# Kernel tuning notes

Measured on AMD Instinct MI355X. Metric: run time of the kernel, lower is better.

The kernel has to match this reference:

```python
import jax, jax.numpy as jnp
import numpy as np

R, DIL = 3, 2  # radius, dilation for neighbor correlation


def conv2d(x, w, b):
    # standard 3x3 stride-1 SAME conv, NCHW / OIHW
    y = jax.lax.conv_general_dilated(x, w, (1, 1), 'SAME',
                                     dimension_numbers=('NCHW', 'OIHW', 'NCHW'))
    return y + b[None, :, None, None]


def bilinear_gather(x, py, px):
    # x: (n,c,h,w); py/px: (n,K,h,w) float sampling coords; zero outside bounds
    n, c, h, w = x.shape
    y0 = jnp.floor(py); x0 = jnp.floor(px)
    wy = py - y0; wx = px - x0
    xf = x.reshape(n, c, h * w)

    def gather(yi, xi):
        valid = ((yi >= 0) & (yi < h) & (xi >= 0) & (xi < w)).astype(x.dtype)
        yc = jnp.clip(yi, 0, h - 1).astype(jnp.int32)
        xc = jnp.clip(xi, 0, w - 1).astype(jnp.int32)
        idx = (yc * w + xc).reshape(n, -1)  # (n, K*h*w)
        v = jax.vmap(lambda f, i: f[:, i])(xf, idx)  # (n, c, K*h*w)
        return v.reshape(n, c, *yi.shape[1:]) * valid[:, None]

    v00 = gather(y0, x0); v01 = gather(y0, x0 + 1)
    v10 = gather(y0 + 1, x0); v11 = gather(y0 + 1, x0 + 1)
    wy_ = wy[:, None]; wx_ = wx[:, None]
    return (v00 * (1 - wy_) * (1 - wx_) + v01 * (1 - wy_) * wx_
            + v10 * wy_ * (1 - wx_) + v11 * wy_ * wx_)


def dcn(x, w, b, ow, ob):
    # DCNv2-style modulated deformable 3x3 conv, stride 1, pad 1, 1 deformable group.
    # Offset/mask predicted by an internal conv: channels = [dy(9), dx(9), mask(9)].
    n, c, h, w_ = x.shape
    K = 9
    om = conv2d(x, ow, ob)  # (n, 27, h, w)
    dy, dx = om[:, :K], om[:, K:2 * K]
    mask = jax.nn.sigmoid(om[:, 2 * K:])
    ky, kx = jnp.meshgrid(jnp.arange(-1, 2), jnp.arange(-1, 2), indexing='ij')
    ky = ky.reshape(K).astype(x.dtype); kx = kx.reshape(K).astype(x.dtype)
    yy = jnp.arange(h, dtype=x.dtype)[None, None, :, None]
    xx = jnp.arange(w_, dtype=x.dtype)[None, None, None, :]
    py = yy + ky[None, :, None, None] + dy  # (n,K,h,w)
    px = xx + kx[None, :, None, None] + dx
    samp = bilinear_gather(x, py, px) * mask[:, None]  # (n,c,K,h,w)
    return jnp.einsum('nckhw,ock->nohw', samp, w.reshape(w.shape[0], c, K)) + b[None, :, None, None]


def ncf(f1, f2, radius, dilation):
    # neighbor_correlation_filter: unfold-based sliding-window dot-product attention
    n, c, h, w = f2.shape
    k = 2 * radius + 1
    pad = (k - 1) * dilation // 2
    f2p = jnp.pad(f2, ((0, 0), (0, 0), (pad, pad), (pad, pad)))
    # (n,c,K,h,w), tap order (ky outer, kx inner) matching F.unfold row-major layout
    patches = jnp.stack([f2p[:, :, i * dilation:i * dilation + h, j * dilation:j * dilation + w]
                         for i in range(k) for j in range(k)], axis=2)
    corr = jnp.einsum('nchw,nckhw->nkhw', f1, patches) / jnp.sqrt(jnp.asarray(c, f1.dtype))
    attn = jax.nn.softmax(corr, axis=1)
    sample = jnp.einsum('nkhw,nckhw->nchw', attn, patches)
    return sample, corr


def stargru(x, t, zw, zb, zow, zob, hw, hb, how, hob):
    tx = jnp.concatenate([x, t], axis=1)
    z = jax.nn.sigmoid(dcn(tx, zw, zb, zow, zob))
    r, _ = ncf(t, x, R, DIL)
    xt = jnp.tanh(dcn(jnp.concatenate([r, t], axis=1), hw, hb, how, hob))
    return (1.0 - z) * t + z * xt


def setup_inputs():
    key = jax.random.key(0)
    N, CIN, CH, H, W = 2, 256, 64, 96, 96
    ks = iter(jax.random.split(key, 32))

    def rn(shape, s=0.05):
        return jax.random.normal(next(ks), shape, jnp.float32) * s

    inp = {
        'x': jax.random.normal(next(ks), (N, CIN, H, W), jnp.float32),
        'template': jax.random.normal(next(ks), (N, CH, H, W), jnp.float32),
        'w_in': rn((CH, CIN, 3, 3)), 'b_in': jnp.zeros((CH,), jnp.float32),
        'w_out': rn((CIN, CH, 3, 3)), 'b_out': jnp.zeros((CIN,), jnp.float32),
    }
    for pre in ('enh_z', 'enh_h', 'upd_z', 'upd_h'):
        inp[pre + '_w'] = rn((CH, 2 * CH, 3, 3))
        inp[pre + '_b'] = jnp.zeros((CH,), jnp.float32)
        inp[pre + '_ow'] = rn((27, 2 * CH, 3, 3), 0.01)  # offset/mask conv (small init)
        inp[pre + '_ob'] = jnp.zeros((27,), jnp.float32)
    return inp


def reference(x, template, w_in, b_in, w_out, b_out,
              enh_z_w, enh_z_b, enh_z_ow, enh_z_ob,
              enh_h_w, enh_h_b, enh_h_ow, enh_h_ob,
              upd_z_w, upd_z_b, upd_z_ow, upd_z_ob,
              upd_h_w, upd_h_b, upd_h_ow, upd_h_ob):
    # CrossUpdate forward, post-first-frame branch (self.template is not None)
    xh = conv2d(x, w_in, b_in)
    x_enh = stargru(template, xh,
                    enh_z_w, enh_z_b, enh_z_ow, enh_z_ob,
                    enh_h_w, enh_h_b, enh_h_ow, enh_h_ob)
    new_template = stargru(xh, template,
                           upd_z_w, upd_z_b, upd_z_ow, upd_z_ob,
                           upd_h_w, upd_h_b, upd_h_ow, upd_h_ob)
    out = conv2d(x_enh, w_out, b_out)
    return (out, new_template)
```

## Files before the change

kernel.cpp:

```cpp
#include <hip/hip_runtime.h>
#include <hip/hip_bf16.h>

typedef __hip_bfloat16 bf16;
typedef unsigned short u16;
typedef unsigned int u32;
typedef __attribute__((ext_vector_type(8))) short short8;
typedef __attribute__((ext_vector_type(4))) short bh4;
typedef __attribute__((ext_vector_type(4))) float floatx4;

constexpr int N_ = 2, H_ = 96, W_ = 96, HW_ = H_ * W_;
constexpr int CIN_ = 256, CH_ = 64, C2_ = 128;

__device__ __forceinline__ float sigm(float v) { return 1.0f / (1.0f + __expf(-v)); }
__device__ __forceinline__ short f2b(float v) { bf16 h = __float2bfloat16(v); return *reinterpret_cast<short*>(&h); }
__device__ __forceinline__ float b2f(short s) {
    union { u32 i; float f; } v; v.i = ((u32)(u16)s) << 16; return v.f;
}

constexpr int A_IN_OFF = 0,                         A_IN_SZ  = 64 * 2304;
constexpr int A_OUT_OFF = A_IN_OFF + A_IN_SZ,       A_OUT_SZ = 256 * 576;
constexpr int A_OFF_OFF = A_OUT_OFF + A_OUT_SZ,     A_OFF_SZ = 64 * 1152;
constexpr int A_DCN_OFF = A_OFF_OFF + 4 * A_OFF_SZ, A_DCN_SZ = 64 * 1152;
constexpr int A_TOT = A_DCN_OFF + 4 * A_DCN_SZ;

__global__ __launch_bounds__(256) void cvt_weights(
        const float* __restrict__ w_in, const float* __restrict__ w_out,
        const float* __restrict__ ow0, const float* __restrict__ ow1,
        const float* __restrict__ ow2, const float* __restrict__ ow3,
        const float* __restrict__ w0, const float* __restrict__ w1,
        const float* __restrict__ w2, const float* __restrict__ w3,
        u16* __restrict__ dst) {
    int id = blockIdx.x * 256 + threadIdx.x;
    if (id >= A_TOT) return;
    float v;
    if (id < A_OUT_OFF) {
        int l = id; int m = l / 2304, k = l % 2304; int tap = k >> 8, ic = k & 255;
        v = w_in[m * 2304 + ic * 9 + tap];
    } else if (id < A_OFF_OFF) {
        int l = id - A_OUT_OFF; int m = l / 576, k = l % 576; int tap = k / 64, ic = k & 63;
        v = w_out[m * 576 + ic * 9 + tap];
    } else if (id < A_DCN_OFF) {
        int l = id - A_OFF_OFF; int i = l / A_OFF_SZ, l2 = l % A_OFF_SZ;
        int m = l2 / 1152, k = l2 % 1152; int tap = k >> 7, ic = k & 127;
        const float* s = (i == 0) ? ow0 : (i == 1) ? ow1 : (i == 2) ? ow2 : ow3;
        v = (m < 27) ? s[m * 1152 + ic * 9 + tap] : 0.f;
    } else {
        int l = id - A_DCN_OFF; int i = l / A_DCN_SZ, l2 = l % A_DCN_SZ;
        int m = l2 / 1152, k = l2 % 1152; int tap = k >> 7, c = k & 127;
        const float* s = (i == 0) ? w0 : (i == 1) ? w1 : (i == 2) ? w2 : w3;
        v = s[m * 1152 + c * 9 + tap];
    }
    short sb = f2b(v);
    dst[id] = *reinterpret_cast<u16*>(&sb);
}

__global__ __launch_bounds__(256) void to_nhwc(const float* __restrict__ src, u16* __restrict__ dst, int C) {
    int id = blockIdx.x * 256 + threadIdx.x;
    int c8n = C >> 3;
    if (id >= N_ * HW_ * c8n) return;
    int c8 = id % c8n;
    int pix = id / c8n;
    int n = pix / HW_, p = pix % HW_;
    const float* s = src + ((size_t)n * C + c8 * 8) * HW_ + p;
    short8 vv;
#pragma unroll
    for (int j = 0; j < 8; ++j) vv[j] = f2b(s[(size_t)j * HW_]);
    *reinterpret_cast<short8*>(dst + (size_t)pix * C + c8 * 8) = vv;
}

__global__ __launch_bounds__(256) void concat_dual(const float* __restrict__ tpl, const float* __restrict__ xh,
                                                   u16* __restrict__ ta, u16* __restrict__ tb) {
    int id = blockIdx.x * 256 + threadIdx.x;
    if (id >= N_ * HW_ * 16) return;
    int c8 = id & 15;
    int pix = id >> 4;
    int n = pix / HW_, p = pix % HW_;
    int c = c8 * 8;
    const float* s = (c < 64) ? tpl + ((size_t)n * 64 + c) * HW_ + p
                              : xh + ((size_t)n * 64 + (c - 64)) * HW_ + p;
    short8 vv;
#pragma unroll
    for (int j = 0; j < 8; ++j) vv[j] = f2b(s[(size_t)j * HW_]);
    *reinterpret_cast<short8*>(ta + (size_t)pix * 128 + c) = vv;
    *reinterpret_cast<short8*>(tb + (size_t)pix * 128 + ((c + 64) & 127)) = vv;
}

template <int IC, int OCST>
__device__ __forceinline__ void conv_core(const u16* __restrict__ X,
                                          const u16* __restrict__ A,
                                          const float* __restrict__ bias,
                                          float* __restrict__ out,
                                          int r, int mt, int t) {
    constexpr int K = IC * 9;
    constexpr int ICC = IC / 64;
    __shared__ __align__(16) u16 Xl[3][50][72];
    int n = r / 192;
    int rr = r % 192;
    int y = rr >> 1, px0 = (rr & 1) * 48;
    int w = t >> 6, lane = t & 63, lm = lane & 15, q = lane >> 4;
    const u16* Arow = A + (size_t)(mt * 64 + w * 16 + lm) * K + q * 8;
    floatx4 acc[3];
#pragma unroll
    for (int a = 0; a < 3; ++a) acc[a] = {0.f, 0.f, 0.f, 0.f};
    const short8 zz = {0, 0, 0, 0, 0, 0, 0, 0};

    for (int icc = 0; icc < ICC; ++icc) {
        short8 af[9][2];
#pragma unroll
        for (int tap = 0; tap < 9; ++tap)
#pragma unroll
            for (int ks = 0; ks < 2; ++ks)
                af[tap][ks] = *reinterpret_cast<const short8*>(Arow + tap * IC + icc * 64 + ks * 32);
        __syncthreads();
#pragma unroll
        for (int it = 0; it < 5; ++it) {
            int id = it * 256 + t;
            if (id < 1200) {
                int ch8 = id & 7;
                int tmp = id >> 3;
                int pxl = tmp % 50, row = tmp / 50;
                int xg = px0 - 1 + pxl;
                int yg = y - 1 + row;
                bool vld = (yg >= 0) && (yg < 96) && (xg >= 0) && (xg < 96);
                short8 vv = zz;
                if (vld)
                    vv = *reinterpret_cast<const short8*>(
                        X + ((size_t)(n * HW_ + yg * 96 + xg)) * IC + icc * 64 + ch8 * 8);
                *reinterpret_cast<short8*>(&Xl[row][pxl][ch8 * 8]) = vv;
            }
        }
        __syncthreads();
#pragma unroll
        for (int tap = 0; tap < 9; ++tap) {
            int ky = tap / 3, kx = tap % 3;
#pragma unroll
            for (int ks = 0; ks < 2; ++ks) {
#pragma unroll
                for (int nf = 0; nf < 3; ++nf) {
                    short8 bv = *reinterpret_cast<const short8*>(&Xl[ky][nf * 16 + lm + kx][ks * 32 + q * 8]);
                    acc[nf] = __builtin_amdgcn_mfma_f32_16x16x32_bf16(af[tap][ks], bv, acc[nf], 0, 0, 0);
                }
            }
        }
    }
    int ocb = mt * 64 + w * 16 + q * 4;
#pragma unroll
    for (int nf = 0; nf < 3; ++nf) {
        int px = px0 + nf * 16 + lm;
#pragma unroll
        for (int rr2 = 0; rr2 < 4; ++rr2) {
            int oc = ocb + rr2;
            if (oc < OCST)
                out[((size_t)(n * OCST + oc)) * HW_ + y * 96 + px] = acc[nf][rr2] + bias[oc];
        }
    }
}

template <int IC, int OCST>
__global__ __launch_bounds__(256) void conv_gemm(const u16* __restrict__ X,
                                                 const u16* __restrict__ A,
                                                 const float* __restrict__ bias,
                                                 float* __restrict__ out) {
    conv_core<IC, OCST>(X, A, bias, out, blockIdx.x % 384, blockIdx.x / 384, threadIdx.x);
}

__global__ __launch_bounds__(256) void conv_gemm2(const u16* __restrict__ X0, const u16* __restrict__ X1,
                                                  const u16* __restrict__ A0, const u16* __restrict__ A1,
                                                  const float* __restrict__ b0, const float* __restrict__ b1,
                                                  float* __restrict__ o0, float* __restrict__ o1) {
    int inst = blockIdx.x / 384, r = blockIdx.x % 384;
    conv_core<C2_, 27>(inst ? X1 : X0, inst ? A1 : A0, inst ? b1 : b0, inst ? o1 : o0, r, 0, threadIdx.x);
}

__device__ __forceinline__ void dcn_core(const u16* __restrict__ txh,
                                         const float* __restrict__ om,
                                         const u16* __restrict__ A,
                                         const float* __restrict__ bias,
                                         float* __restrict__ out,
                                         int r, int t) {
    __shared__ __align__(16) u16 Bl[48][72];
    __shared__ float s_wy[432], s_wx[432], s_m[432];
    __shared__ int s_y0[432], s_x0[432];
    int n = r / 192;
    int rr = r % 192;
    int y = rr >> 1, px0 = (rr & 1) * 48;
    for (int e = t; e < 432; e += 256) {
        int k9 = e / 48, xl = e % 48;
        int x = px0 + xl;
        const float* ob = om + (size_t)n * 27 * HW_ + y * 96 + x;
        float dy = ob[(size_t)k9 * HW_];
        float dx = ob[(size_t)(9 + k9) * HW_];
        float ml = ob[(size_t)(18 + k9) * HW_];
        float py = (float)y + (float)(k9 / 3 - 1) + dy;
        float px = (float)x + (float)(k9 % 3 - 1) + dx;
        float fy = floorf(py), fx = floorf(px);
        s_y0[e] = (int)fy; s_x0[e] = (int)fx;
        s_wy[e] = py - fy; s_wx[e] = px - fx; s_m[e] = sigm(ml);
    }
    int w = t >> 6, lane = t & 63, lm = lane & 15, q = lane >> 4;
    const u16* Arow = A + (size_t)(w * 16 + lm) * 1152 + q * 8;
    floatx4 acc[3];
#pragma unroll
    for (int a = 0; a < 3; ++a) acc[a] = {0.f, 0.f, 0.f, 0.f};
    const u16* txn = txh + (size_t)n * HW_ * 128;
    const short8 zz = {0, 0, 0, 0, 0, 0, 0, 0};

    for (int kc = 0; kc < 18; ++kc) {
        int tap = kc >> 1, c0 = (kc & 1) * 64;
        short8 af[2];
#pragma unroll
        for (int ks = 0; ks < 2; ++ks)
            af[ks] = *reinterpret_cast<const short8*>(Arow + kc * 64 + ks * 32);
        __syncthreads();
#pragma unroll
        for (int i = 0; i < 2; ++i) {
            int id = i * 256 + t;
            if (id < 384) {
                int px = id >> 3, ch8 = id & 7;
                int ce = tap * 48 + px;
                int y0 = s_y0[ce], x0 = s_x0[ce];
                float wy = s_wy[ce], wx = s_wx[ce], m = s_m[ce];
                float w00 = (1.f - wy) * (1.f - wx) * m;
                float w01 = (1.f - wy) * wx * m;
                float w10 = wy * (1.f - wx) * m;
                float w11 = wy * wx * m;
                bool yv0 = (y0 >= 0) & (y0 < 96), yv1 = (y0 >= -1) & (y0 < 95);
                bool xv0 = (x0 >= 0) & (x0 < 96), xv1 = (x0 >= -1) & (x0 < 95);
                const u16* base = txn + (long)(y0 * 96 + x0) * 128 + c0 + ch8 * 8;
                short8 v00 = (yv0 && xv0) ? *reinterpret_cast<const short8*>(base) : zz;
                short8 v01 = (yv0 && xv1) ? *reinterpret_cast<const short8*>(base + 128) : zz;
                short8 v10 = (yv1 && xv0) ? *reinterpret_cast<const short8*>(base + 96 * 128) : zz;
                short8 v11 = (yv1 && xv1) ? *reinterpret_cast<const short8*>(base + 96 * 128 + 128) : zz;
                short8 vv;
#pragma unroll
                for (int j = 0; j < 8; ++j) {
                    float f = b2f(v00[j]) * w00 + b2f(v01[j]) * w01 +
                              b2f(v10[j]) * w10 + b2f(v11[j]) * w11;
                    vv[j] = f2b(f);
                }
                *reinterpret_cast<short8*>(&Bl[px][ch8 * 8]) = vv;
            }
        }
        __syncthreads();
#pragma unroll
        for (int ks = 0; ks < 2; ++ks)
#pragma unroll
            for (int nf = 0; nf < 3; ++nf) {
                short8 bv = *reinterpret_cast<const short8*>(&Bl[nf * 16 + lm][ks * 32 + q * 8]);
                acc[nf] = __builtin_amdgcn_mfma_f32_16x16x32_bf16(af[ks], bv, acc[nf], 0, 0, 0);
            }
    }
    int ocb = w * 16 + q * 4;
#pragma unroll
    for (int nf = 0; nf < 3; ++nf) {
        int px = px0 + nf * 16 + lm;
#pragma unroll
        for (int rr2 = 0; rr2 < 4; ++rr2) {
            int oc = ocb + rr2;
            out[((size_t)(n * CH_ + oc)) * HW_ + y * 96 + px] = acc[nf][rr2] + bias[oc];
        }
    }
}

__global__ __launch_bounds__(256) void dcn_gemm2(const u16* __restrict__ X0, const u16* __restrict__ X1,
                                                 const float* __restrict__ om0, const float* __restrict__ om1,
                                                 const u16* __restrict__ A0, const u16* __restrict__ A1,
                                                 const float* __restrict__ b0, const float* __restrict__ b1,
                                                 float* __restrict__ o0, float* __restrict__ o1) {
    int inst = blockIdx.x / 384, r = blockIdx.x % 384;
    dcn_core(inst ? X1 : X0, inst ? om1 : om0, inst ? A1 : A0, inst ? b1 : b0, inst ? o1 : o0, r, threadIdx.x);
}

__global__ __launch_bounds__(256, 4) void ncf2(const u16* __restrict__ in0, const u16* __restrict__ in1,
                                               u16* __restrict__ out0, u16* __restrict__ out1) {
    __shared__ __align__(16) u16 sF2[7][28][72];
    __shared__ __align__(16) u16 sF1[16][72];
    __shared__ float sc[16][52];
    int t = threadIdx.x;
    int inst = blockIdx.x / 1152, bb = blockIdx.x % 1152;
    const u16* txh = inst ? in1 : in0;
    u16* txh2 = inst ? out1 : out0;
    int n = bb / 576, rem = bb % 576;
    int y = rem / 6, x0 = (rem % 6) * 16;
    const u16* base = txh + (size_t)n * HW_ * 128;
    const short8 zz = {0, 0, 0, 0, 0, 0, 0, 0};

    for (int id = t; id < 1568; id += 256) {
        int ch8 = id & 7;
        int tmp = id >> 3;
        int px = tmp % 28, row = tmp / 28;
        int yy = y + row * 2 - 6;
        int xg = x0 - 6 + px;
        short8 vv = zz;
        if (yy >= 0 && yy < 96 && xg >= 0 && xg < 96)
            vv = *reinterpret_cast<const short8*>(base + (size_t)(yy * 96 + xg) * 128 + ch8 * 8);
        *reinterpret_cast<short8*>(&sF2[row][px][ch8 * 8]) = vv;
    }
    if (t < 128) {
        int ch8 = t & 7, lp0 = t >> 3;
        short8 vv = *reinterpret_cast<const short8*>(base + (size_t)(y * 96 + x0 + lp0) * 128 + 64 + ch8 * 8);
        *reinterpret_cast<short8*>(&sF1[lp0][ch8 * 8]) = vv;
    }
    __syncthreads();

    int lp = t >> 4, j = t & 15;
    for (int k = j; k < 49; k += 16) {
        int ky = k / 7, kx = k % 7;
        const u16* f2p = &sF2[ky][lp + 2 * kx][0];
        const u16* f1p = &sF1[lp][0];
        float s = 0.f;
#pragma unroll
        for (int c8 = 0; c8 < 8; ++c8) {
            short8 a = *reinterpret_cast<const short8*>(f1p + c8 * 8);
            short8 b = *reinterpret_cast<const short8*>(f2p + c8 * 8);
#pragma unroll
            for (int u = 0; u < 8; ++u) s += b2f(a[u]) * b2f(b[u]);
        }
        sc[lp][k] = s * 0.125f;
    }
    float mx = -1e30f;
    for (int k = j; k < 49; k += 16) mx = fmaxf(mx, sc[lp][k]);
#pragma unroll
    for (int m = 1; m <= 8; m <<= 1) mx = fmaxf(mx, __shfl_xor(mx, m, 64));
    float e[4];
    float sum = 0.f;
    int cnt = 0;
    for (int k = j; k < 49; k += 16) { e[cnt] = __expf(sc[lp][k] - mx); sum += e[cnt]; ++cnt; }
#pragma unroll
    for (int m = 1; m <= 8; m <<= 1) sum += __shfl_xor(sum, m, 64);
    float inv = 1.f / sum;
    cnt = 0;
    for (int k = j; k < 49; k += 16) sc[lp][k] = e[cnt++] * inv;
    __syncthreads();
    int ch0 = j * 4;
    float acc[4];
#pragma unroll
    for (int u = 0; u < 4; ++u) acc[u] = 0.f;
#pragma unroll
    for (int k = 0; k < 49; ++k) {
        int ky = k / 7, kx = k % 7;
        float a = sc[lp][k];
        bh4 f2 = *reinterpret_cast<const bh4*>(&sF2[ky][lp + 2 * kx][ch0]);
#pragma unroll
        for (int u = 0; u < 4; ++u) acc[u] += a * b2f(f2[u]);
    }
    int p = y * 96 + x0 + lp;
    u16* obase = txh2 + (size_t)n * HW_ * 128 + (size_t)p * 128;
    bh4 ro;
#pragma unroll
    for (int u = 0; u < 4; ++u) ro[u] = f2b(acc[u]);
    *reinterpret_cast<bh4*>(obase + ch0) = ro;
    *reinterpret_cast<bh4*>(obase + 64 + ch0) =
        *reinterpret_cast<const bh4*>(&sF1[lp][ch0]);
}

__global__ __launch_bounds__(256) void gate_dual(const float* __restrict__ dz_a, const float* __restrict__ dh_a,
                                                 const float* __restrict__ t_a, u16* __restrict__ dst_a,
                                                 const float* __restrict__ dz_b, const float* __restrict__ dh_b,
                                                 const float* __restrict__ t_b, float* __restrict__ dst_b) {
    int inst = blockIdx.x / 576, bb = blockIdx.x % 576;
    int id = bb * 256 + threadIdx.x;
    int c8 = id & 7;
    int pix = id >> 3;
    int n = pix / HW_, p = pix % HW_;
    const float* zpre = inst ? dz_b : dz_a;
    const float* hpre = inst ? dh_b : dh_a;
    const float* tt = inst ? t_b : t_a;
    if (!inst) {
        short8 vv;
#pragma unroll
        for (int j = 0; j < 8; ++j) {
            size_t idx = ((size_t)n * CH_ + c8 * 8 + j) * HW_ + p;
            float z = sigm(zpre[idx]);
            float xt = tanhf(hpre[idx]);
            vv[j] = f2b((1.f - z) * tt[idx] + z * xt);
        }
        *reinterpret_cast<short8*>(dst_a + (size_t)pix * CH_ + c8 * 8) = vv;
    } else {
#pragma unroll
        for (int j = 0; j < 8; ++j) {
            size_t idx = ((size_t)n * CH_ + c8 * 8 + j) * HW_ + p;
            float z = sigm(zpre[idx]);
            float xt = tanhf(hpre[idx]);
            dst_b[idx] = (1.f - z) * tt[idx] + z * xt;
        }
    }
}

extern "C" void kernel_launch(void* const* d_in, const int* in_sizes, int n_in,
                              void* d_out, int out_size, void* d_ws, size_t ws_size,
                              hipStream_t stream) {
    const float* x     = (const float*)d_in[0];
    const float* tpl   = (const float*)d_in[1];
    const float* w_in  = (const float*)d_in[2];
    const float* b_in  = (const float*)d_in[3];
    const float* w_out = (const float*)d_in[4];
    const float* b_out = (const float*)d_in[5];
    const float *pw[4], *pb[4], *pow_[4], *pob[4];
    for (int i = 0; i < 4; ++i) {
        pw[i]   = (const float*)d_in[6 + 4 * i];
        pb[i]   = (const float*)d_in[7 + 4 * i];
        pow_[i] = (const float*)d_in[8 + 4 * i];
        pob[i]  = (const float*)d_in[9 + 4 * i];
    }
    float* out_main = (float*)d_out;
    float* out_ntpl = out_main + (size_t)N_ * CIN_ * HW_;

    u16* Aws = (u16*)d_ws;
    u16* xT     = Aws + A_TOT;
    u16* txh_a  = xT + (size_t)N_ * HW_ * CIN_;
    u16* txh_b  = txh_a + (size_t)N_ * HW_ * C2_;
    u16* txh2_a = txh_b + (size_t)N_ * HW_ * C2_;
    u16* txh2_b = txh2_a + (size_t)N_ * HW_ * C2_;
    u16* xeh    = txh2_b + (size_t)N_ * HW_ * C2_;
    float* fws = (float*)(xeh + (size_t)N_ * HW_ * CH_);
    size_t off = 0;
    float* xh   = fws + off; off += (size_t)N_ * CH_ * HW_;
    float* om_a = fws + off; off += (size_t)N_ * 27 * HW_;
    float* om_b = fws + off; off += (size_t)N_ * 27 * HW_;
    float* dz_a = fws + off; off += (size_t)N_ * CH_ * HW_;
    float* dz_b = fws + off; off += (size_t)N_ * CH_ * HW_;
    float* dh_a = fws + off; off += (size_t)N_ * CH_ * HW_;
    float* dh_b = fws + off; off += (size_t)N_ * CH_ * HW_;

    cvt_weights<<<(A_TOT + 255) / 256, 256, 0, stream>>>(
        w_in, w_out, pow_[0], pow_[1], pow_[2], pow_[3], pw[0], pw[1], pw[2], pw[3], Aws);
    to_nhwc<<<2304, 256, 0, stream>>>(x, xT, CIN_);
    conv_gemm<CIN_, 64><<<384, 256, 0, stream>>>(xT, Aws + A_IN_OFF, b_in, xh);

    concat_dual<<<1152, 256, 0, stream>>>(tpl, xh, txh_a, txh_b);
    conv_gemm2<<<768, 256, 0, stream>>>(txh_a, txh_b,
        Aws + A_OFF_OFF + 0 * A_OFF_SZ, Aws + A_OFF_OFF + 2 * A_OFF_SZ, pob[0], pob[2], om_a, om_b);
    dcn_gemm2<<<768, 256, 0, stream>>>(txh_a, txh_b, om_a, om_b,
        Aws + A_DCN_OFF + 0 * A_DCN_SZ, Aws + A_DCN_OFF + 2 * A_DCN_SZ, pb[0], pb[2], dz_a, dz_b);
    ncf2<<<2304, 256, 0, stream>>>(txh_a, txh_b, txh2_a, txh2_b);
    conv_gemm2<<<768, 256, 0, stream>>>(txh2_a, txh2_b,
        Aws + A_OFF_OFF + 1 * A_OFF_SZ, Aws + A_OFF_OFF + 3 * A_OFF_SZ, pob[1], pob[3], om_a, om_b);
    dcn_gemm2<<<768, 256, 0, stream>>>(txh2_a, txh2_b, om_a, om_b,
        Aws + A_DCN_OFF + 1 * A_DCN_SZ, Aws + A_DCN_OFF + 3 * A_DCN_SZ, pb[1], pb[3], dh_a, dh_b);
    gate_dual<<<1152, 256, 0, stream>>>(dz_a, dh_a, xh, xeh, dz_b, dh_b, tpl, out_ntpl);

    conv_gemm<CH_, 256><<<1536, 256, 0, stream>>>(xeh, Aws + A_OUT_OFF, b_out, out_main);
}
```

Baseline: 344.0 us.

## Shrink conv/DCN tiles to 32 pixels and merge four offset-conv/DCN launches

The conv and DCN GEMM cores now cover 32-pixel row segments instead of 48, giving more blocks per launch and a smaller LDS footprint. The separate enhance and update offset-conv and DCN launches become one four-instance conv_quad and one dcn_quad launch, with ncf2 moved ahead so all inputs are ready. This cuts launch count and fixes under-filled grids on a large-CU GPU. In exchange, halo overhead per pixel rises (34/32 vs 50/48), weight fragment reuse per block drops, and a second pair of offset buffers is needed.

```diff
diff --git a/kernel.cpp b/kernel.cpp
--- a/kernel.cpp
+++ b/kernel.cpp
@@ -93,15 +93,15 @@
                                           int r, int mt, int t) {
     constexpr int K = IC * 9;
     constexpr int ICC = IC / 64;
-    __shared__ __align__(16) u16 Xl[3][50][72];
-    int n = r / 192;
-    int rr = r % 192;
-    int y = rr >> 1, px0 = (rr & 1) * 48;
+    __shared__ __align__(16) u16 Xl[3][34][72];
+    int n = r / 288;
+    int rr = r % 288;
+    int y = rr / 3, px0 = (rr % 3) * 32;
     int w = t >> 6, lane = t & 63, lm = lane & 15, q = lane >> 4;
     const u16* Arow = A + (size_t)(mt * 64 + w * 16 + lm) * K + q * 8;
-    floatx4 acc[3];
-#pragma unroll
-    for (int a = 0; a < 3; ++a) acc[a] = {0.f, 0.f, 0.f, 0.f};
+    floatx4 acc[2];
+#pragma unroll
+    for (int a = 0; a < 2; ++a) acc[a] = {0.f, 0.f, 0.f, 0.f};
     const short8 zz = {0, 0, 0, 0, 0, 0, 0, 0};
 
     for (int icc = 0; icc < ICC; ++icc) {
@@ -113,12 +113,12 @@
                 af[tap][ks] = *reinterpret_cast<const short8*>(Arow + tap * IC + icc * 64 + ks * 32);
         __syncthreads();
 #pragma unroll
-        for (int it = 0; it < 5; ++it) {
+        for (int it = 0; it < 4; ++it) {
             int id = it * 256 + t;
-            if (id < 1200) {
+            if (id < 816) {
                 int ch8 = id & 7;
                 int tmp = id >> 3;
-                int pxl = tmp % 50, row = tmp / 50;
+                int pxl = tmp % 34, row = tmp / 34;
                 int xg = px0 - 1 + pxl;
                 int yg = y - 1 + row;
                 bool vld = (yg >= 0) && (yg < 96) && (xg >= 0) && (xg < 96);
@@ -136,7 +136,7 @@
 #pragma unroll
             for (int ks = 0; ks < 2; ++ks) {
 #pragma unroll
-                for (int nf = 0; nf < 3; ++nf) {
+                for (int nf = 0; nf < 2; ++nf) {
                     short8 bv = *reinterpret_cast<const short8*>(&Xl[ky][nf * 16 + lm + kx][ks * 32 + q * 8]);
                     acc[nf] = __builtin_amdgcn_mfma_f32_16x16x32_bf16(af[tap][ks], bv, acc[nf], 0, 0, 0);
                 }
@@ -145,7 +145,7 @@
     }
     int ocb = mt * 64 + w * 16 + q * 4;
 #pragma unroll
-    for (int nf = 0; nf < 3; ++nf) {
+    for (int nf = 0; nf < 2; ++nf) {
         int px = px0 + nf * 16 + lm;
 #pragma unroll
         for (int rr2 = 0; rr2 < 4; ++rr2) {
@@ -161,15 +161,23 @@
                                                  const u16* __restrict__ A,
                                                  const float* __restrict__ bias,
                                                  float* __restrict__ out) {
-    conv_core<IC, OCST>(X, A, bias, out, blockIdx.x % 384, blockIdx.x / 384, threadIdx.x);
-}
-
-__global__ __launch_bounds__(256) void conv_gemm2(const u16* __restrict__ X0, const u16* __restrict__ X1,
-                                                  const u16* __restrict__ A0, const u16* __restrict__ A1,
-                                                  const float* __restrict__ b0, const float* __restrict__ b1,
-                                                  float* __restrict__ o0, float* __restrict__ o1) {
-    int inst = blockIdx.x / 384, r = blockIdx.x % 384;
-    conv_core<C2_, 27>(inst ? X1 : X0, inst ? A1 : A0, inst ? b1 : b0, inst ? o1 : o0, r, 0, threadIdx.x);
+    conv_core<IC, OCST>(X, A, bias, out, blockIdx.x % 576, blockIdx.x / 576, threadIdx.x);
+}
+
+__global__ __launch_bounds__(256) void conv_quad(const u16* __restrict__ X0, const u16* __restrict__ X1,
+                                                 const u16* __restrict__ X2, const u16* __restrict__ X3,
+                                                 const u16* __restrict__ A0, const u16* __restrict__ A1,
+                                                 const u16* __restrict__ A2, const u16* __restrict__ A3,
+                                                 const float* __restrict__ b0, const float* __restrict__ b1,
+                                                 const float* __restrict__ b2, const float* __restrict__ b3,
+                                                 float* __restrict__ o0, float* __restrict__ o1,
+                                                 float* __restrict__ o2, float* __restrict__ o3) {
+    int inst = blockIdx.x / 576, r = blockIdx.x % 576;
+    const u16* X = (inst == 0) ? X0 : (inst == 1) ? X1 : (inst == 2) ? X2 : X3;
+    const u16* A = (inst == 0) ? A0 : (inst == 1) ? A1 : (inst == 2) ? A2 : A3;
+    const float* b = (inst == 0) ? b0 : (inst == 1) ? b1 : (inst == 2) ? b2 : b3;
+    float* o = (inst == 0) ? o0 : (inst == 1) ? o1 : (inst == 2) ? o2 : o3;
+    conv_core<C2_, 27>(X, A, b, o, r, 0, threadIdx.x);
 }
 
 __device__ __forceinline__ void dcn_core(const u16* __restrict__ txh,
@@ -178,14 +186,14 @@
                                          const float* __restrict__ bias,
                                          float* __restrict__ out,
                                          int r, int t) {
-    __shared__ __align__(16) u16 Bl[48][72];
-    __shared__ float s_wy[432], s_wx[432], s_m[432];
-    __shared__ int s_y0[432], s_x0[432];
-    int n = r / 192;
-    int rr = r % 192;
-    int y = rr >> 1, px0 = (rr & 1) * 48;
-    for (int e = t; e < 432; e += 256) {
-        int k9 = e / 48, xl = e % 48;
+    __shared__ __align__(16) u16 Bl[32][72];
+    __shared__ float s_wy[288], s_wx[288], s_m[288];
+    __shared__ int s_y0[288], s_x0[288];
+    int n = r / 288;
+    int rr = r % 288;
+    int y = rr / 3, px0 = (rr % 3) * 32;
+    for (int e = t; e < 288; e += 256) {
+        int k9 = e / 32, xl = e % 32;
         int x = px0 + xl;
         const float* ob = om + (size_t)n * 27 * HW_ + y * 96 + x;
         float dy = ob[(size_t)k9 * HW_];
@@ -199,9 +207,9 @@
     }
     int w = t >> 6, lane = t & 63, lm = lane & 15, q = lane >> 4;
     const u16* Arow = A + (size_t)(w * 16 + lm) * 1152 + q * 8;
-    floatx4 acc[3];
-#pragma unroll
-    for (int a = 0; a < 3; ++a) acc[a] = {0.f, 0.f, 0.f, 0.f};
+    floatx4 acc[2];
+#pragma unroll
+    for (int a = 0; a < 2; ++a) acc[a] = {0.f, 0.f, 0.f, 0.f};
     const u16* txn = txh + (size_t)n * HW_ * 128;
     const short8 zz = {0, 0, 0, 0, 0, 0, 0, 0};
 
@@ -212,47 +220,43 @@
         for (int ks = 0; ks < 2; ++ks)
             af[ks] = *reinterpret_cast<const short8*>(Arow + kc * 64 + ks * 32);
         __syncthreads();
-#pragma unroll
-        for (int i = 0; i < 2; ++i) {
-            int id = i * 256 + t;
-            if (id < 384) {
-                int px = id >> 3, ch8 = id & 7;
-                int ce = tap * 48 + px;
-                int y0 = s_y0[ce], x0 = s_x0[ce];
-                float wy = s_wy[ce], wx = s_wx[ce], m = s_m[ce];
-                float w00 = (1.f - wy) * (1.f - wx) * m;
-                float w01 = (1.f - wy) * wx * m;
-                float w10 = wy * (1.f - wx) * m;
-                float w11 = wy * wx * m;
-                bool yv0 = (y0 >= 0) & (y0 < 96), yv1 = (y0 >= -1) & (y0 < 95);
-                bool xv0 = (x0 >= 0) & (x0 < 96), xv1 = (x0 >= -1) & (x0 < 95);
-                const u16* base = txn + (long)(y0 * 96 + x0) * 128 + c0 + ch8 * 8;
-                short8 v00 = (yv0 && xv0) ? *reinterpret_cast<const short8*>(base) : zz;
-                short8 v01 = (yv0 && xv1) ? *reinterpret_cast<const short8*>(base + 128) : zz;
-                short8 v10 = (yv1 && xv0) ? *reinterpret_cast<const short8*>(base + 96 * 128) : zz;
-                short8 v11 = (yv1 && xv1) ? *reinterpret_cast<const short8*>(base + 96 * 128 + 128) : zz;
-                short8 vv;
-#pragma unroll
-                for (int j = 0; j < 8; ++j) {
-                    float f = b2f(v00[j]) * w00 + b2f(v01[j]) * w01 +
-                              b2f(v10[j]) * w10 + b2f(v11[j]) * w11;
-                    vv[j] = f2b(f);
-                }
-                *reinterpret_cast<short8*>(&Bl[px][ch8 * 8]) = vv;
+        {
+            int px = t >> 3, ch8 = t & 7;
+            int ce = tap * 32 + px;
+            int y0 = s_y0[ce], x0 = s_x0[ce];
+            float wy = s_wy[ce], wx = s_wx[ce], m = s_m[ce];
+            float w00 = (1.f - wy) * (1.f - wx) * m;
+            float w01 = (1.f - wy) * wx * m;
+            float w10 = wy * (1.f - wx) * m;
+            float w11 = wy * wx * m;
+            bool yv0 = (y0 >= 0) & (y0 < 96), yv1 = (y0 >= -1) & (y0 < 95);
+            bool xv0 = (x0 >= 0) & (x0 < 96), xv1 = (x0 >= -1) & (x0 < 95);
+            const u16* base = txn + (long)(y0 * 96 + x0) * 128 + c0 + ch8 * 8;
+            short8 v00 = (yv0 && xv0) ? *reinterpret_cast<const short8*>(base) : zz;
+            short8 v01 = (yv0 && xv1) ? *reinterpret_cast<const short8*>(base + 128) : zz;
+            short8 v10 = (yv1 && xv0) ? *reinterpret_cast<const short8*>(base + 96 * 128) : zz;
+            short8 v11 = (yv1 && xv1) ? *reinterpret_cast<const short8*>(base + 96 * 128 + 128) : zz;
+            short8 vv;
+#pragma unroll
+            for (int j = 0; j < 8; ++j) {
+                float f = b2f(v00[j]) * w00 + b2f(v01[j]) * w01 +
+                          b2f(v10[j]) * w10 + b2f(v11[j]) * w11;
+                vv[j] = f2b(f);
             }
+            *reinterpret_cast<short8*>(&Bl[px][ch8 * 8]) = vv;
         }
         __syncthreads();
 #pragma unroll
         for (int ks = 0; ks < 2; ++ks)
 #pragma unroll
-            for (int nf = 0; nf < 3; ++nf) {
+            for (int nf = 0; nf < 2; ++nf) {
                 short8 bv = *reinterpret_cast<const short8*>(&Bl[nf * 16 + lm][ks * 32 + q * 8]);
                 acc[nf] = __builtin_amdgcn_mfma_f32_16x16x32_bf16(af[ks], bv, acc[nf], 0, 0, 0);
             }
     }
     int ocb = w * 16 + q * 4;
 #pragma unroll
-    for (int nf = 0; nf < 3; ++nf) {
+    for (int nf = 0; nf < 2; ++nf) {
         int px = px0 + nf * 16 + lm;
 #pragma unroll
         for (int rr2 = 0; rr2 < 4; ++rr2) {
@@ -262,13 +266,23 @@
     }
 }
 
-__global__ __launch_bounds__(256) void dcn_gemm2(const u16* __restrict__ X0, const u16* __restrict__ X1,
-                                                 const float* __restrict__ om0, const float* __restrict__ om1,
-                                                 const u16* __restrict__ A0, const u16* __restrict__ A1,
-                                                 const float* __restrict__ b0, const float* __restrict__ b1,
-                                                 float* __restrict__ o0, float* __restrict__ o1) {
-    int inst = blockIdx.x / 384, r = blockIdx.x % 384;
-    dcn_core(inst ? X1 : X0, inst ? om1 : om0, inst ? A1 : A0, inst ? b1 : b0, inst ? o1 : o0, r, threadIdx.x);
+__global__ __launch_bounds__(256) void dcn_quad(const u16* __restrict__ X0, const u16* __restrict__ X1,
+                                                const u16* __restrict__ X2, const u16* __restrict__ X3,
+                                                const float* __restrict__ om0, const float* __restrict__ om1,
+                                                const float* __restrict__ om2, const float* __restrict__ om3,
+                                                const u16* __restrict__ A0, const u16* __restrict__ A1,
+                                                const u16* __restrict__ A2, const u16* __restrict__ A3,
+                                                const float* __restrict__ b0, const float* __restrict__ b1,
+                                                const float* __restrict__ b2, const float* __restrict__ b3,
+                                                float* __restrict__ o0, float* __restrict__ o1,
+                                                float* __restrict__ o2, float* __restrict__ o3) {
+    int inst = blockIdx.x / 576, r = blockIdx.x % 576;
+    const u16* X = (inst == 0) ? X0 : (inst == 1) ? X1 : (inst == 2) ? X2 : X3;
+    const float* om = (inst == 0) ? om0 : (inst == 1) ? om1 : (inst == 2) ? om2 : om3;
+    const u16* A = (inst == 0) ? A0 : (inst == 1) ? A1 : (inst == 2) ? A2 : A3;
+    const float* b = (inst == 0) ? b0 : (inst == 1) ? b1 : (inst == 2) ? b2 : b3;
+    float* o = (inst == 0) ? o0 : (inst == 1) ? o1 : (inst == 2) ? o2 : o3;
+    dcn_core(X, om, A, b, o, r, threadIdx.x);
 }
 
 __global__ __launch_bounds__(256, 4) void ncf2(const u16* __restrict__ in0, const u16* __restrict__ in1,
@@ -416,8 +430,10 @@
     float* fws = (float*)(xeh + (size_t)N_ * HW_ * CH_);
     size_t off = 0;
     float* xh   = fws + off; off += (size_t)N_ * CH_ * HW_;
-    float* om_a = fws + off; off += (size_t)N_ * 27 * HW_;
-    float* om_b = fws + off; off += (size_t)N_ * 27 * HW_;
+    float* om0  = fws + off; off += (size_t)N_ * 27 * HW_;
+    float* om1  = fws + off; off += (size_t)N_ * 27 * HW_;
+    float* om2  = fws + off; off += (size_t)N_ * 27 * HW_;
+    float* om3  = fws + off; off += (size_t)N_ * 27 * HW_;
     float* dz_a = fws + off; off += (size_t)N_ * CH_ * HW_;
     float* dz_b = fws + off; off += (size_t)N_ * CH_ * HW_;
     float* dh_a = fws + off; off += (size_t)N_ * CH_ * HW_;
@@ -426,19 +442,21 @@
     cvt_weights<<<(A_TOT + 255) / 256, 256, 0, stream>>>(
         w_in, w_out, pow_[0], pow_[1], pow_[2], pow_[3], pw[0], pw[1], pw[2], pw[3], Aws);
     to_nhwc<<<2304, 256, 0, stream>>>(x, xT, CIN_);
-    conv_gemm<CIN_, 64><<<384, 256, 0, stream>>>(xT, Aws + A_IN_OFF, b_in, xh);
+    conv_gemm<CIN_, 64><<<576, 256, 0, stream>>>(xT, Aws + A_IN_OFF, b_in, xh);
 
     concat_dual<<<1152, 256, 0, stream>>>(tpl, xh, txh_a, txh_b);
-    conv_gemm2<<<768, 256, 0, stream>>>(txh_a, txh_b,
-        Aws + A_OFF_OFF + 0 * A_OFF_SZ, Aws + A_OFF_OFF + 2 * A_OFF_SZ, pob[0], pob[2], om_a, om_b);
-    dcn_gemm2<<<768, 256, 0, stream>>>(txh_a, txh_b, om_a, om_b,
-        Aws + A_DCN_OFF + 0 * A_DCN_SZ, Aws + A_DCN_OFF + 2 * A_DCN_SZ, pb[0], pb[2], dz_a, dz_b);
     ncf2<<<2304, 256, 0, stream>>>(txh_a, txh_b, txh2_a, txh2_b);
-    conv_gemm2<<<768, 256, 0, stream>>>(txh2_a, txh2_b,
-        Aws + A_OFF_OFF + 1 * A_OFF_SZ, Aws + A_OFF_OFF + 3 * A_OFF_SZ, pob[1], pob[3], om_a, om_b);
-    dcn_gemm2<<<768, 256, 0, stream>>>(txh2_a, txh2_b, om_a, om_b,
-        Aws + A_DCN_OFF + 1 * A_DCN_SZ, Aws + A_DCN_OFF + 3 * A_DCN_SZ, pb[1], pb[3], dh_a, dh_b);
+    conv_quad<<<2304, 256, 0, stream>>>(
+        txh_a, txh_b, txh2_a, txh2_b,
+        Aws + A_OFF_OFF + 0 * A_OFF_SZ, Aws + A_OFF_OFF + 2 * A_OFF_SZ,
+        Aws + A_OFF_OFF + 1 * A_OFF_SZ, Aws + A_OFF_OFF + 3 * A_OFF_SZ,
+        pob[0], pob[2], pob[1], pob[3], om0, om1, om2, om3);
+    dcn_quad<<<2304, 256, 0, stream>>>(
+        txh_a, txh_b, txh2_a, txh2_b, om0, om1, om2, om3,
+        Aws + A_DCN_OFF + 0 * A_DCN_SZ, Aws + A_DCN_OFF + 2 * A_DCN_SZ,
+        Aws + A_DCN_OFF + 1 * A_DCN_SZ, Aws + A_DCN_OFF + 3 * A_DCN_SZ,
+        pb[0], pb[2], pb[1], pb[3], dz_a, dz_b, dh_a, dh_b);
     gate_dual<<<1152, 256, 0, stream>>>(dz_a, dh_a, xh, xeh, dz_b, dh_b, tpl, out_ntpl);
 
-    conv_gemm<CH_, 256><<<1536, 256, 0, stream>>>(xeh, Aws + A_OUT_OFF, b_out, out_main);
-}
+    conv_gemm<CH_, 256><<<2304, 256, 0, stream>>>(xeh, Aws + A_OUT_OFF, b_out, out_main);
+}
```

New measurement: 349.5 us. About the same (+1.6%).
